# Kernel optimization log

Measured on AMD Instinct MI355X. Metric: run time of the kernel, lower is better.

The kernel has to match this reference:

```python
import jax, jax.numpy as jnp
import numpy as np

B, S, D, H, DFF = 2, 2048, 1024, 16, 4096
DK = D // H
EPS = 1e-5

def setup_inputs() -> dict:
    key = jax.random.key(0)
    ks = jax.random.split(key, 8)
    sc = lambda n: 1.0 / np.sqrt(n)
    return {
        "x": jax.random.normal(ks[0], (B, S, D), dtype=jnp.float32),
        "g1": jnp.ones((D,), dtype=jnp.float32),
        "g2": jnp.ones((D,), dtype=jnp.float32),
        "wq": jax.random.normal(ks[1], (D, D), dtype=jnp.float32) * sc(D),
        "wk": jax.random.normal(ks[2], (D, D), dtype=jnp.float32) * sc(D),
        "wv": jax.random.normal(ks[3], (D, D), dtype=jnp.float32) * sc(D),
        "wo": jax.random.normal(ks[4], (D, D), dtype=jnp.float32) * sc(D),
        "w1": jax.random.normal(ks[5], (DFF, D), dtype=jnp.float32) * sc(D),
        "w2": jax.random.normal(ks[6], (D, DFF), dtype=jnp.float32) * sc(DFF),
    }

def rmsnorm(a, g):
    norm = jnp.sqrt(jnp.mean(a * a, axis=-1, keepdims=True) + EPS)
    return a / norm * g

def gelu_erf(x):
    return x * 0.5 * (1.0 + jax.lax.erf(x * (1.0 / np.sqrt(2.0))))

def reference(x, g1, g2, wq, wk, wv, wo, w1, w2):
    b, s, d = x.shape
    h, dk = H, DK
    # --- attention sublayer (pre-norm) ---
    xn = rmsnorm(x, g1)
    # nn.Linear: y = x @ W.T ; reshape to [b, h, s, dk]
    q = (xn @ wq.T).reshape(b, s, h, dk).transpose(0, 2, 1, 3)
    k = (xn @ wk.T).reshape(b, s, h, dk).transpose(0, 2, 1, 3)
    v = (xn @ wv.T).reshape(b, s, h, dk).transpose(0, 2, 1, 3)
    scores = jnp.einsum('bhqd,bhkd->bhqk', q, k) / np.sqrt(dk).astype(np.float32)
    causal = jnp.triu(jnp.ones((s, s), dtype=bool), k=1)  # True above diagonal -> masked
    scores = jnp.where(causal, -jnp.inf, scores)
    weights = jax.nn.softmax(scores, axis=-1)
    attn = jnp.einsum('bhqk,bhkd->bhqd', weights, v)
    attn = attn.transpose(0, 2, 1, 3).reshape(b, s, d)
    x = x + attn @ wo.T
    # --- FFN sublayer (pre-norm) ---
    xn2 = rmsnorm(x, g2)
    ff = gelu_erf(xn2 @ w1.T) @ w2.T
    return x + ff
```

## Files before the change

### kernel.cpp

```cpp
#include <hip/hip_runtime.h>
#include <hip/hip_bf16.h>

typedef __attribute__((ext_vector_type(8))) short bf16x8;
typedef __attribute__((ext_vector_type(4))) float f32x4;

__device__ __forceinline__ unsigned short f2b(float f) {
    unsigned int u = __float_as_uint(f);
    unsigned int r = u + 0x7FFFu + ((u >> 16) & 1u);
    return (unsigned short)(r >> 16);
}

__device__ __forceinline__ float gelu_erf(float v) {
    return 0.5f * v * (1.0f + erff(v * 0.70710678118654752f));
}

__device__ __forceinline__ void gload_lds16(const void* g, void* l) {
    __builtin_amdgcn_global_load_lds(
        (const __attribute__((address_space(1))) void*)g,
        (__attribute__((address_space(3))) void*)l, 16, 0, 0);
}

__global__ void cast_bf16_k(const float* __restrict__ src, unsigned short* __restrict__ dst, int n4) {
    int i = blockIdx.x * blockDim.x + threadIdx.x;
    if (i < n4) {
        float4 v = ((const float4*)src)[i];
        ushort4 o;
        o.x = f2b(v.x); o.y = f2b(v.y); o.z = f2b(v.z); o.w = f2b(v.w);
        ((ushort4*)dst)[i] = o;
    }
}

__global__ void rmsnorm_bf16_k(const float* __restrict__ x, const float* __restrict__ g,
                               unsigned short* __restrict__ out) {
    int row = blockIdx.x;
    int t = threadIdx.x;
    const float4* xr = (const float4*)(x + (size_t)row * 1024);
    float4 xv = xr[t];
    float ss = xv.x * xv.x + xv.y * xv.y + xv.z * xv.z + xv.w * xv.w;
    #pragma unroll
    for (int off = 32; off; off >>= 1) ss += __shfl_xor(ss, off, 64);
    __shared__ float red[4];
    int wave = t >> 6, lane = t & 63;
    if (lane == 0) red[wave] = ss;
    __syncthreads();
    float tot = red[0] + red[1] + red[2] + red[3];
    float rn = rsqrtf(tot * (1.0f / 1024.0f) + 1e-5f);
    float4 gv = ((const float4*)g)[t];
    ushort4 o4;
    o4.x = f2b(xv.x * rn * gv.x);
    o4.y = f2b(xv.y * rn * gv.y);
    o4.z = f2b(xv.z * rn * gv.z);
    o4.w = f2b(xv.w * rn * gv.w);
    ((ushort4*)out)[(size_t)row * 256 + t] = o4;
}

__global__ void vtrans_k(const unsigned short* __restrict__ qkv, unsigned short* __restrict__ vt) {
    __shared__ unsigned short Ls[64 * 72];
    int st = blockIdx.x, bh = blockIdx.y, b = bh >> 4, h = bh & 15;
    int s0 = st * 64;
    int tid = threadIdx.x;
    const unsigned short* Vg = qkv + (size_t)(b * 2048 + s0) * 3072 + 2048 + h * 64;
    #pragma unroll
    for (int i = 0; i < 2; i++) {
        int idx = i * 256 + tid;
        int r = idx >> 3, c8 = (idx & 7) * 8;
        *(uint4*)&Ls[r * 72 + c8] = *(const uint4*)&Vg[(size_t)r * 3072 + c8];
    }
    __syncthreads();
    #pragma unroll
    for (int i = 0; i < 2; i++) {
        int idx = i * 256 + tid;
        int d = idx >> 3, s8 = (idx & 7) * 8;
        unsigned short tmp[8];
        #pragma unroll
        for (int j = 0; j < 8; j++) tmp[j] = Ls[(s8 + j) * 72 + d];
        *(uint4*)&vt[(size_t)(bh * 64 + d) * 2048 + s0 + s8] = *(uint4*)tmp;
    }
}

template <int EPI>
__launch_bounds__(256)
__global__ void gemm_bt(const unsigned short* __restrict__ A, const unsigned short* __restrict__ B,
                        const float* __restrict__ res, void* __restrict__ out,
                        int M, int N, int K) {
    __shared__ __align__(16) unsigned short smem[2 * 128 * 32];
    unsigned short* As = smem;
    unsigned short* Bs = smem + 128 * 32;

    int tid = threadIdx.x;
    int wave = tid >> 6, lane = tid & 63;
    int lrow = lane & 15, quad = lane >> 4;
    int qx8 = (quad ^ ((lrow >> 1) & 3)) * 8;

    int gx = gridDim.x, gy = gridDim.y;
    int cid = blockIdx.y * gx + blockIdx.x;
    int per = (gx * gy) >> 3;
    int nid = (cid & 7) * per + (cid >> 3);
    const int CG = 8;
    int group = nid / (CG * gy);
    int rem = nid % (CG * gy);
    int bxs = group * CG + (rem % CG);
    int bys = rem / CG;
    int bm = bys * 128, bn = bxs * 128;

    int wm = (wave & 1) * 64, wn = (wave >> 1) * 64;

    const unsigned short* Ab = A + (size_t)bm * K;
    const unsigned short* Bb = B + (size_t)bn * K;

    f32x4 zero = {0.f, 0.f, 0.f, 0.f};
    f32x4 acc[4][4];
    #pragma unroll
    for (int mi = 0; mi < 4; mi++)
        #pragma unroll
        for (int ni = 0; ni < 4; ni++) acc[mi][ni] = zero;

    int wbase = tid & 192;

    for (int k0 = 0; k0 < K; k0 += 32) {
        if (k0) __syncthreads();
        #pragma unroll
        for (int i = 0; i < 2; i++) {
            int idx = i * 256 + tid;
            int r = idx >> 2;
            int c = ((idx & 3) ^ ((idx >> 3) & 3)) * 8;
            gload_lds16(&Ab[(size_t)r * K + k0 + c], As + ((size_t)(i * 256 + wbase)) * 8);
            gload_lds16(&Bb[(size_t)r * K + k0 + c], Bs + ((size_t)(i * 256 + wbase)) * 8);
        }
        __syncthreads();

        bf16x8 af[4], bfr[4];
        #pragma unroll
        for (int mi = 0; mi < 4; mi++)
            af[mi] = *(const bf16x8*)&As[(wm + mi * 16 + lrow) * 32 + qx8];
        #pragma unroll
        for (int ni = 0; ni < 4; ni++)
            bfr[ni] = *(const bf16x8*)&Bs[(wn + ni * 16 + lrow) * 32 + qx8];
        #pragma unroll
        for (int mi = 0; mi < 4; mi++)
            #pragma unroll
            for (int ni = 0; ni < 4; ni++)
                acc[mi][ni] = __builtin_amdgcn_mfma_f32_16x16x32_bf16(af[mi], bfr[ni], acc[mi][ni], 0, 0, 0);
    }

    float* Cs = (float*)smem;
    int row16 = lane >> 2, cseg = (lane & 3) * 16;
    #pragma unroll
    for (int p = 0; p < 4; p++) {
        __syncthreads();
        #pragma unroll
        for (int ni = 0; ni < 4; ni++)
            #pragma unroll
            for (int r = 0; r < 4; r++)
                Cs[wave * 1024 + (quad * 4 + r) * 64 + ni * 16 + lrow] = acc[p][ni][r];
        __syncthreads();
        const float* src = &Cs[wave * 1024 + row16 * 64 + cseg];
        int grow = bm + wm + p * 16 + row16;
        int gcol = bn + wn + cseg;
        size_t off = (size_t)grow * N + gcol;
        if (EPI == 1) {
            float* op = (float*)out + off;
            const float* rp = res + off;
            #pragma unroll
            for (int j = 0; j < 4; j++) {
                float4 v = ((const float4*)src)[j];
                float4 rr = ((const float4*)rp)[j];
                v.x += rr.x; v.y += rr.y; v.z += rr.z; v.w += rr.w;
                ((float4*)op)[j] = v;
            }
        } else {
            unsigned short tmp[16];
            #pragma unroll
            for (int j = 0; j < 16; j++) {
                float v = src[j];
                if (EPI == 2) v = gelu_erf(v);
                tmp[j] = f2b(v);
            }
            unsigned short* op = (unsigned short*)out + off;
            *(uint4*)op = *(uint4*)tmp;
            *(uint4*)(op + 8) = *(uint4*)(tmp + 8);
        }
    }
}

__launch_bounds__(256)
__global__ void gemm_bt64(const unsigned short* __restrict__ A, const unsigned short* __restrict__ B,
                          const float* __restrict__ res, float* __restrict__ out,
                          int M, int N, int K) {
    __shared__ __align__(16) unsigned short As[128 * 32];
    __shared__ __align__(16) unsigned short Bs[64 * 32];

    int tid = threadIdx.x, wave = tid >> 6, lane = tid & 63;
    int lrow = lane & 15, quad = lane >> 4;
    int qx8 = (quad ^ ((lrow >> 1) & 3)) * 8;

    int gx = gridDim.x, gy = gridDim.y;
    int cid = blockIdx.y * gx + blockIdx.x;
    int per = (gx * gy) >> 3;
    int nid = (cid & 7) * per + (cid >> 3);
    const int CG = 8;
    int group = nid / (CG * gy);
    int rem = nid % (CG * gy);
    int bxs = group * CG + (rem % CG);
    int bys = rem / CG;
    int bm = bys * 128, bn = bxs * 64;

    int wm = (wave & 1) * 64, wn = (wave >> 1) * 32;

    f32x4 zero = {0.f, 0.f, 0.f, 0.f};
    f32x4 acc[4][2];
    #pragma unroll
    for (int mi = 0; mi < 4; mi++)
        #pragma unroll
        for (int ni = 0; ni < 2; ni++) acc[mi][ni] = zero;

    int rr4 = lane >> 2;
    int c8s = ((lane & 3) ^ ((lane >> 3) & 3)) * 8;
    const unsigned short* Ab = A + (size_t)(bm + wave * 32 + rr4) * K + c8s;
    const unsigned short* Bb = B + (size_t)(bn + wave * 16 + rr4) * K + c8s;

    for (int k0 = 0; k0 < K; k0 += 32) {
        if (k0) __syncthreads();
        gload_lds16(Ab + k0, &As[(wave * 32) * 32]);
        gload_lds16(Ab + (size_t)16 * K + k0, &As[(wave * 32 + 16) * 32]);
        gload_lds16(Bb + k0, &Bs[(wave * 16) * 32]);
        __syncthreads();

        bf16x8 af[4], bfr[2];
        #pragma unroll
        for (int mi = 0; mi < 4; mi++)
            af[mi] = *(const bf16x8*)&As[(wm + mi * 16 + lrow) * 32 + qx8];
        #pragma unroll
        for (int ni = 0; ni < 2; ni++)
            bfr[ni] = *(const bf16x8*)&Bs[(wn + ni * 16 + lrow) * 32 + qx8];
        #pragma unroll
        for (int mi = 0; mi < 4; mi++)
            #pragma unroll
            for (int ni = 0; ni < 2; ni++)
                acc[mi][ni] = __builtin_amdgcn_mfma_f32_16x16x32_bf16(af[mi], bfr[ni], acc[mi][ni], 0, 0, 0);
    }

    float* Cs = (float*)As;
    int row16 = lane >> 2, cseg = (lane & 3) * 8;
    #pragma unroll
    for (int p = 0; p < 4; p++) {
        __syncthreads();
        #pragma unroll
        for (int ni = 0; ni < 2; ni++)
            #pragma unroll
            for (int r = 0; r < 4; r++)
                Cs[wave * 512 + (quad * 4 + r) * 32 + ni * 16 + lrow] = acc[p][ni][r];
        __syncthreads();
        const float* src = &Cs[wave * 512 + row16 * 32 + cseg];
        int grow = bm + wm + p * 16 + row16;
        int gcol = bn + wn + cseg;
        size_t off = (size_t)grow * N + gcol;
        float* op = out + off;
        const float* rp = res + off;
        #pragma unroll
        for (int j = 0; j < 2; j++) {
            float4 v = ((const float4*)src)[j];
            float4 rv = ((const float4*)rp)[j];
            v.x += rv.x; v.y += rv.y; v.z += rv.z; v.w += rv.w;
            ((float4*)op)[j] = v;
        }
    }
}

__launch_bounds__(256)
__global__ void attn_k(const unsigned short* __restrict__ qkv,
                       const unsigned short* __restrict__ vt,
                       unsigned short* __restrict__ attn_out) {
    const int ROWQKV = 3072;
    int qt = (int)(gridDim.x - 1 - blockIdx.x);
    int bh = blockIdx.y;
    int b = bh >> 4, h = bh & 15;
    int q0 = qt * 128;

    __shared__ __align__(16) unsigned short Ks[2][2][64 * 32];
    __shared__ __align__(16) unsigned short Vs[2][2][64 * 32];
    __shared__ __align__(16) unsigned short Ps[8][16 * 72];

    int tid = threadIdx.x, wave = tid >> 6, lane = tid & 63;
    int lrow = lane & 15, quad = lane >> 4;
    int rr4 = lane >> 2;
    int c8s = ((lane & 3) ^ ((lane >> 3) & 3)) * 8;
    int qx8 = (quad ^ ((lrow >> 1) & 3)) * 8;

    size_t base = (size_t)b * 2048 * ROWQKV;

    const unsigned short* QgA = qkv + base + (size_t)(q0 + wave * 16 + lrow) * ROWQKV + h * 64 + quad * 8;
    bf16x8 aA0 = *(const bf16x8*)QgA;
    bf16x8 aA1 = *(const bf16x8*)(QgA + 32);
    const unsigned short* QgB = QgA + (size_t)64 * ROWQKV;
    bf16x8 aB0 = *(const bf16x8*)QgB;
    bf16x8 aB1 = *(const bf16x8*)(QgB + 32);

    const unsigned short* Kg0 = qkv + base + (size_t)(wave * 16 + rr4) * ROWQKV + 1024 + h * 64 + c8s;
    const unsigned short* Vg0 = vt + (size_t)(bh * 64 + wave * 16 + rr4) * 2048 + c8s;

    f32x4 zero = {0.f, 0.f, 0.f, 0.f};
    f32x4 oA[4], oB[4];
    float lA[4], lB[4];
    #pragma unroll
    for (int ni = 0; ni < 4; ni++) { oA[ni] = zero; oB[ni] = zero; }
    #pragma unroll
    for (int r = 0; r < 4; r++) { lA[r] = 0.f; lB[r] = 0.f; }

    const float C = 0.18033688011112042f;

    unsigned short* PwA = Ps[wave];
    unsigned short* PwB = Ps[wave + 4];

    gload_lds16(Kg0,      &Ks[0][0][wave * 16 * 32]);
    gload_lds16(Kg0 + 32, &Ks[0][1][wave * 16 * 32]);
    gload_lds16(Vg0,      &Vs[0][0][wave * 16 * 32]);
    gload_lds16(Vg0 + 32, &Vs[0][1][wave * 16 * 32]);

    auto process = [&](bf16x8 a0, bf16x8 a1, f32x4* o, float* l,
                       unsigned short* Pw, bool diag, int buf) {
        f32x4 s[4];
        #pragma unroll
        for (int ni = 0; ni < 4; ni++) s[ni] = zero;
        #pragma unroll
        for (int ni = 0; ni < 4; ni++) {
            bf16x8 bb = *(const bf16x8*)&Ks[buf][0][(ni * 16 + lrow) * 32 + qx8];
            s[ni] = __builtin_amdgcn_mfma_f32_16x16x32_bf16(a0, bb, s[ni], 0, 0, 0);
        }
        #pragma unroll
        for (int ni = 0; ni < 4; ni++) {
            bf16x8 bb = *(const bf16x8*)&Ks[buf][1][(ni * 16 + lrow) * 32 + qx8];
            s[ni] = __builtin_amdgcn_mfma_f32_16x16x32_bf16(a1, bb, s[ni], 0, 0, 0);
        }
        if (diag) {
            #pragma unroll
            for (int r = 0; r < 4; r++)
                #pragma unroll
                for (int ni = 0; ni < 4; ni++) {
                    float p = exp2f(s[ni][r] * C);
                    if (ni * 16 + lrow > wave * 16 + quad * 4 + r) p = 0.f;
                    s[ni][r] = p;
                    l[r] += p;
                }
        } else {
            #pragma unroll
            for (int r = 0; r < 4; r++)
                #pragma unroll
                for (int ni = 0; ni < 4; ni++) {
                    float p = exp2f(s[ni][r] * C);
                    s[ni][r] = p;
                    l[r] += p;
                }
        }
        #pragma unroll
        for (int ni = 0; ni < 4; ni++)
            #pragma unroll
            for (int r = 0; r < 4; r++)
                Pw[(quad * 4 + r) * 72 + ni * 16 + lrow] = f2b(s[ni][r]);
        bf16x8 p0 = *(const bf16x8*)&Pw[lrow * 72 + quad * 8];
        bf16x8 p1 = *(const bf16x8*)&Pw[lrow * 72 + 32 + quad * 8];
        #pragma unroll
        for (int ni = 0; ni < 4; ni++) {
            bf16x8 bb = *(const bf16x8*)&Vs[buf][0][(ni * 16 + lrow) * 32 + qx8];
            o[ni] = __builtin_amdgcn_mfma_f32_16x16x32_bf16(p0, bb, o[ni], 0, 0, 0);
        }
        #pragma unroll
        for (int ni = 0; ni < 4; ni++) {
            bf16x8 bb = *(const bf16x8*)&Vs[buf][1][(ni * 16 + lrow) * 32 + qx8];
            o[ni] = __builtin_amdgcn_mfma_f32_16x16x32_bf16(p1, bb, o[ni], 0, 0, 0);
        }
    };

    int nkt = 2 * qt + 2;
    for (int kt = 0; kt < nkt; kt++) {
        __syncthreads();
        if (kt + 1 < nkt) {
            int nb = (kt + 1) & 1;
            const unsigned short* Kg = Kg0 + (size_t)(kt + 1) * 64 * ROWQKV;
            const unsigned short* Vg = Vg0 + (size_t)(kt + 1) * 64;
            gload_lds16(Kg,      &Ks[nb][0][wave * 16 * 32]);
            gload_lds16(Kg + 32, &Ks[nb][1][wave * 16 * 32]);
            gload_lds16(Vg,      &Vs[nb][0][wave * 16 * 32]);
            gload_lds16(Vg + 32, &Vs[nb][1][wave * 16 * 32]);
        }
        int buf = kt & 1;
        if (kt < nkt - 1) process(aA0, aA1, oA, lA, PwA, kt == nkt - 2, buf);
        process(aB0, aB1, oB, lB, PwB, kt == nkt - 1, buf);
    }

    #pragma unroll
    for (int r = 0; r < 4; r++) {
        #pragma unroll
        for (int off = 1; off < 16; off <<= 1) {
            lA[r] += __shfl_xor(lA[r], off, 64);
            lB[r] += __shfl_xor(lB[r], off, 64);
        }
    }

    #pragma unroll
    for (int strip = 0; strip < 2; strip++) {
        f32x4* o = strip ? oB : oA;
        float* l = strip ? lB : lA;
        #pragma unroll
        for (int r = 0; r < 4; r++) {
            float inv = 1.0f / l[r];
            int q = q0 + strip * 64 + wave * 16 + quad * 4 + r;
            #pragma unroll
            for (int ni = 0; ni < 4; ni++)
                attn_out[((size_t)b * 2048 + q) * 1024 + h * 64 + ni * 16 + lrow] = f2b(o[ni][r] * inv);
        }
    }
}

extern "C" void kernel_launch(void* const* d_in, const int* in_sizes, int n_in,
                              void* d_out, int out_size, void* d_ws, size_t ws_size,
                              hipStream_t stream) {
    const float* x  = (const float*)d_in[0];
    const float* g1 = (const float*)d_in[1];
    const float* g2 = (const float*)d_in[2];
    const float* wq = (const float*)d_in[3];
    const float* wk = (const float*)d_in[4];
    const float* wv = (const float*)d_in[5];
    const float* wo = (const float*)d_in[6];
    const float* w1 = (const float*)d_in[7];
    const float* w2 = (const float*)d_in[8];
    float* out = (float*)d_out;

    const size_t BS = 4096;
    const size_t D = 1024, DFF = 4096;

    char* w = (char*)d_ws;
    unsigned short* xn_b   = (unsigned short*)w; w += BS * D * 2;
    unsigned short* wqkv_b = (unsigned short*)w; w += 3 * D * D * 2;
    unsigned short* qkv_b  = (unsigned short*)w; w += BS * 3 * D * 2;
    unsigned short* vt_b   = (unsigned short*)w; w += BS * D * 2;
    unsigned short* attn_b = (unsigned short*)w; w += BS * D * 2;
    unsigned short* wo_b   = (unsigned short*)w; w += D * D * 2;
    float*          x2     = (float*)w;          w += BS * D * 4;
    unsigned short* xn2_b  = (unsigned short*)w; w += BS * D * 2;
    unsigned short* w1_b   = (unsigned short*)w; w += DFF * D * 2;
    unsigned short* h_b    = (unsigned short*)w; w += BS * DFF * 2;
    unsigned short* w2_b   = (unsigned short*)w; w += D * DFF * 2;

    int nW = (int)(D * D / 4);
    cast_bf16_k<<<(nW + 255) / 256, 256, 0, stream>>>(wq, wqkv_b, nW);
    cast_bf16_k<<<(nW + 255) / 256, 256, 0, stream>>>(wk, wqkv_b + D * D, nW);
    cast_bf16_k<<<(nW + 255) / 256, 256, 0, stream>>>(wv, wqkv_b + 2 * D * D, nW);
    cast_bf16_k<<<(nW + 255) / 256, 256, 0, stream>>>(wo, wo_b, nW);
    int nF = (int)(DFF * D / 4);
    cast_bf16_k<<<(nF + 255) / 256, 256, 0, stream>>>(w1, w1_b, nF);
    cast_bf16_k<<<(nF + 255) / 256, 256, 0, stream>>>(w2, w2_b, nF);

    rmsnorm_bf16_k<<<(int)BS, 256, 0, stream>>>(x, g1, xn_b);

    gemm_bt<0><<<dim3(24, 32), 256, 0, stream>>>(xn_b, wqkv_b, nullptr, qkv_b, 4096, 3072, 1024);

    vtrans_k<<<dim3(32, 32), 256, 0, stream>>>(qkv_b, vt_b);

    attn_k<<<dim3(16, 32), 256, 0, stream>>>(qkv_b, vt_b, attn_b);

    gemm_bt64<<<dim3(16, 32), 256, 0, stream>>>(attn_b, wo_b, x, x2, 4096, 1024, 1024);

    rmsnorm_bf16_k<<<(int)BS, 256, 0, stream>>>(x2, g2, xn2_b);

    gemm_bt<2><<<dim3(32, 32), 256, 0, stream>>>(xn2_b, w1_b, nullptr, h_b, 4096, 4096, 1024);

    gemm_bt64<<<dim3(16, 32), 256, 0, stream>>>(h_b, w2_b, x2, out, 4096, 1024, 4096);
}
```

Before: 393.4 us.

## Load attention K/V fragments directly from global, halve query tile, fold scale into Wq

```diff
diff --git a/kernel.cpp b/kernel.cpp
--- a/kernel.cpp
+++ b/kernel.cpp
@@ -20,12 +20,14 @@
         (__attribute__((address_space(3))) void*)l, 16, 0, 0);
 }
 
-__global__ void cast_bf16_k(const float* __restrict__ src, unsigned short* __restrict__ dst, int n4) {
+__global__ void cast_bf16_k(const float* __restrict__ src, unsigned short* __restrict__ dst,
+                            int n4, float scale) {
     int i = blockIdx.x * blockDim.x + threadIdx.x;
     if (i < n4) {
         float4 v = ((const float4*)src)[i];
         ushort4 o;
-        o.x = f2b(v.x); o.y = f2b(v.y); o.z = f2b(v.z); o.w = f2b(v.w);
+        o.x = f2b(v.x * scale); o.y = f2b(v.y * scale);
+        o.z = f2b(v.z * scale); o.w = f2b(v.w * scale);
         ((ushort4*)dst)[i] = o;
     }
 }
@@ -275,140 +277,108 @@
     int qt = (int)(gridDim.x - 1 - blockIdx.x);
     int bh = blockIdx.y;
     int b = bh >> 4, h = bh & 15;
-    int q0 = qt * 128;
-
-    __shared__ __align__(16) unsigned short Ks[2][2][64 * 32];
-    __shared__ __align__(16) unsigned short Vs[2][2][64 * 32];
-    __shared__ __align__(16) unsigned short Ps[8][16 * 72];
+    int q0 = qt * 64;
+
+    __shared__ __align__(16) unsigned short Ps[4][16 * 72];
 
     int tid = threadIdx.x, wave = tid >> 6, lane = tid & 63;
     int lrow = lane & 15, quad = lane >> 4;
-    int rr4 = lane >> 2;
-    int c8s = ((lane & 3) ^ ((lane >> 3) & 3)) * 8;
-    int qx8 = (quad ^ ((lrow >> 1) & 3)) * 8;
 
     size_t base = (size_t)b * 2048 * ROWQKV;
 
-    const unsigned short* QgA = qkv + base + (size_t)(q0 + wave * 16 + lrow) * ROWQKV + h * 64 + quad * 8;
-    bf16x8 aA0 = *(const bf16x8*)QgA;
-    bf16x8 aA1 = *(const bf16x8*)(QgA + 32);
-    const unsigned short* QgB = QgA + (size_t)64 * ROWQKV;
-    bf16x8 aB0 = *(const bf16x8*)QgB;
-    bf16x8 aB1 = *(const bf16x8*)(QgB + 32);
-
-    const unsigned short* Kg0 = qkv + base + (size_t)(wave * 16 + rr4) * ROWQKV + 1024 + h * 64 + c8s;
-    const unsigned short* Vg0 = vt + (size_t)(bh * 64 + wave * 16 + rr4) * 2048 + c8s;
+    const unsigned short* Qg = qkv + base + (size_t)(q0 + wave * 16 + lrow) * ROWQKV + h * 64 + quad * 8;
+    bf16x8 qf0 = *(const bf16x8*)Qg;
+    bf16x8 qf1 = *(const bf16x8*)(Qg + 32);
+
+    const unsigned short* Kg = qkv + base + (size_t)lrow * ROWQKV + 1024 + h * 64 + quad * 8;
+    const unsigned short* Vg = vt + (size_t)(bh * 64 + lrow) * 2048 + quad * 8;
 
     f32x4 zero = {0.f, 0.f, 0.f, 0.f};
-    f32x4 oA[4], oB[4];
-    float lA[4], lB[4];
-    #pragma unroll
-    for (int ni = 0; ni < 4; ni++) { oA[ni] = zero; oB[ni] = zero; }
-    #pragma unroll
-    for (int r = 0; r < 4; r++) { lA[r] = 0.f; lB[r] = 0.f; }
-
-    const float C = 0.18033688011112042f;
-
-    unsigned short* PwA = Ps[wave];
-    unsigned short* PwB = Ps[wave + 4];
-
-    gload_lds16(Kg0,      &Ks[0][0][wave * 16 * 32]);
-    gload_lds16(Kg0 + 32, &Ks[0][1][wave * 16 * 32]);
-    gload_lds16(Vg0,      &Vs[0][0][wave * 16 * 32]);
-    gload_lds16(Vg0 + 32, &Vs[0][1][wave * 16 * 32]);
-
-    auto process = [&](bf16x8 a0, bf16x8 a1, f32x4* o, float* l,
-                       unsigned short* Pw, bool diag, int buf) {
+    f32x4 o[4];
+    #pragma unroll
+    for (int ni = 0; ni < 4; ni++) o[ni] = zero;
+    float l = 0.f;
+
+    unsigned short* Pw = Ps[wave];
+    int qloc = wave * 16 + lrow;
+
+    for (int kt = 0; kt <= qt; kt++) {
+        const unsigned short* Kt = Kg + (size_t)(kt * 64) * ROWQKV;
+        const unsigned short* Vt = Vg + kt * 64;
+
+        bf16x8 kf[4][2];
+        #pragma unroll
+        for (int ni = 0; ni < 4; ni++) {
+            kf[ni][0] = *(const bf16x8*)(Kt + (size_t)(ni * 16) * ROWQKV);
+            kf[ni][1] = *(const bf16x8*)(Kt + (size_t)(ni * 16) * ROWQKV + 32);
+        }
+        bf16x8 vf[4][2];
+        #pragma unroll
+        for (int ni = 0; ni < 4; ni++) {
+            vf[ni][0] = *(const bf16x8*)(Vt + (size_t)(ni * 16) * 2048);
+            vf[ni][1] = *(const bf16x8*)(Vt + (size_t)(ni * 16) * 2048 + 32);
+        }
+
         f32x4 s[4];
         #pragma unroll
         for (int ni = 0; ni < 4; ni++) s[ni] = zero;
         #pragma unroll
-        for (int ni = 0; ni < 4; ni++) {
-            bf16x8 bb = *(const bf16x8*)&Ks[buf][0][(ni * 16 + lrow) * 32 + qx8];
-            s[ni] = __builtin_amdgcn_mfma_f32_16x16x32_bf16(a0, bb, s[ni], 0, 0, 0);
-        }
-        #pragma unroll
-        for (int ni = 0; ni < 4; ni++) {
-            bf16x8 bb = *(const bf16x8*)&Ks[buf][1][(ni * 16 + lrow) * 32 + qx8];
-            s[ni] = __builtin_amdgcn_mfma_f32_16x16x32_bf16(a1, bb, s[ni], 0, 0, 0);
-        }
-        if (diag) {
-            #pragma unroll
-            for (int r = 0; r < 4; r++)
+        for (int ni = 0; ni < 4; ni++)
+            s[ni] = __builtin_amdgcn_mfma_f32_16x16x32_bf16(kf[ni][0], qf0, s[ni], 0, 0, 0);
+        #pragma unroll
+        for (int ni = 0; ni < 4; ni++)
+            s[ni] = __builtin_amdgcn_mfma_f32_16x16x32_bf16(kf[ni][1], qf1, s[ni], 0, 0, 0);
+
+        if (kt == qt) {
+            #pragma unroll
+            for (int ni = 0; ni < 4; ni++)
                 #pragma unroll
-                for (int ni = 0; ni < 4; ni++) {
-                    float p = exp2f(s[ni][r] * C);
-                    if (ni * 16 + lrow > wave * 16 + quad * 4 + r) p = 0.f;
+                for (int r = 0; r < 4; r++) {
+                    float p = exp2f(s[ni][r]);
+                    if (ni * 16 + quad * 4 + r > qloc) p = 0.f;
                     s[ni][r] = p;
-                    l[r] += p;
+                    l += p;
                 }
         } else {
             #pragma unroll
-            for (int r = 0; r < 4; r++)
+            for (int ni = 0; ni < 4; ni++)
                 #pragma unroll
-                for (int ni = 0; ni < 4; ni++) {
-                    float p = exp2f(s[ni][r] * C);
+                for (int r = 0; r < 4; r++) {
+                    float p = exp2f(s[ni][r]);
                     s[ni][r] = p;
-                    l[r] += p;
+                    l += p;
                 }
         }
-        #pragma unroll
-        for (int ni = 0; ni < 4; ni++)
-            #pragma unroll
-            for (int r = 0; r < 4; r++)
-                Pw[(quad * 4 + r) * 72 + ni * 16 + lrow] = f2b(s[ni][r]);
+
+        #pragma unroll
+        for (int ni = 0; ni < 4; ni++) {
+            uint2 pk;
+            pk.x = (unsigned int)f2b(s[ni][0]) | ((unsigned int)f2b(s[ni][1]) << 16);
+            pk.y = (unsigned int)f2b(s[ni][2]) | ((unsigned int)f2b(s[ni][3]) << 16);
+            *(uint2*)&Pw[lrow * 72 + ni * 16 + quad * 4] = pk;
+        }
         bf16x8 p0 = *(const bf16x8*)&Pw[lrow * 72 + quad * 8];
         bf16x8 p1 = *(const bf16x8*)&Pw[lrow * 72 + 32 + quad * 8];
-        #pragma unroll
-        for (int ni = 0; ni < 4; ni++) {
-            bf16x8 bb = *(const bf16x8*)&Vs[buf][0][(ni * 16 + lrow) * 32 + qx8];
-            o[ni] = __builtin_amdgcn_mfma_f32_16x16x32_bf16(p0, bb, o[ni], 0, 0, 0);
-        }
-        #pragma unroll
-        for (int ni = 0; ni < 4; ni++) {
-            bf16x8 bb = *(const bf16x8*)&Vs[buf][1][(ni * 16 + lrow) * 32 + qx8];
-            o[ni] = __builtin_amdgcn_mfma_f32_16x16x32_bf16(p1, bb, o[ni], 0, 0, 0);
-        }
-    };
-
-    int nkt = 2 * qt + 2;
-    for (int kt = 0; kt < nkt; kt++) {
-        __syncthreads();
-        if (kt + 1 < nkt) {
-            int nb = (kt + 1) & 1;
-            const unsigned short* Kg = Kg0 + (size_t)(kt + 1) * 64 * ROWQKV;
-            const unsigned short* Vg = Vg0 + (size_t)(kt + 1) * 64;
-            gload_lds16(Kg,      &Ks[nb][0][wave * 16 * 32]);
-            gload_lds16(Kg + 32, &Ks[nb][1][wave * 16 * 32]);
-            gload_lds16(Vg,      &Vs[nb][0][wave * 16 * 32]);
-            gload_lds16(Vg + 32, &Vs[nb][1][wave * 16 * 32]);
-        }
-        int buf = kt & 1;
-        if (kt < nkt - 1) process(aA0, aA1, oA, lA, PwA, kt == nkt - 2, buf);
-        process(aB0, aB1, oB, lB, PwB, kt == nkt - 1, buf);
-    }
+
+        #pragma unroll
+        for (int ni = 0; ni < 4; ni++)
+            o[ni] = __builtin_amdgcn_mfma_f32_16x16x32_bf16(p0, vf[ni][0], o[ni], 0, 0, 0);
+        #pragma unroll
+        for (int ni = 0; ni < 4; ni++)
+            o[ni] = __builtin_amdgcn_mfma_f32_16x16x32_bf16(p1, vf[ni][1], o[ni], 0, 0, 0);
+    }
+
+    l += __shfl_xor(l, 16, 64);
+    l += __shfl_xor(l, 32, 64);
 
     #pragma unroll
     for (int r = 0; r < 4; r++) {
-        #pragma unroll
-        for (int off = 1; off < 16; off <<= 1) {
-            lA[r] += __shfl_xor(lA[r], off, 64);
-            lB[r] += __shfl_xor(lB[r], off, 64);
-        }
-    }
-
-    #pragma unroll
-    for (int strip = 0; strip < 2; strip++) {
-        f32x4* o = strip ? oB : oA;
-        float* l = strip ? lB : lA;
-        #pragma unroll
-        for (int r = 0; r < 4; r++) {
-            float inv = 1.0f / l[r];
-            int q = q0 + strip * 64 + wave * 16 + quad * 4 + r;
-            #pragma unroll
-            for (int ni = 0; ni < 4; ni++)
-                attn_out[((size_t)b * 2048 + q) * 1024 + h * 64 + ni * 16 + lrow] = f2b(o[ni][r] * inv);
-        }
+        float lr = __shfl(l, quad * 4 + r, 64);
+        float inv = 1.0f / lr;
+        int q = q0 + wave * 16 + quad * 4 + r;
+        #pragma unroll
+        for (int ni = 0; ni < 4; ni++)
+            attn_out[((size_t)b * 2048 + q) * 1024 + h * 64 + ni * 16 + lrow] = f2b(o[ni][r] * inv);
     }
 }
 
@@ -428,6 +398,7 @@
 
     const size_t BS = 4096;
     const size_t D = 1024, DFF = 4096;
+    const float QSCALE = 0.18033688011112042f;
 
     char* w = (char*)d_ws;
     unsigned short* xn_b   = (unsigned short*)w; w += BS * D * 2;
@@ -443,13 +414,13 @@
     unsigned short* w2_b   = (unsigned short*)w; w += D * DFF * 2;
 
     int nW = (int)(D * D / 4);
-    cast_bf16_k<<<(nW + 255) / 256, 256, 0, stream>>>(wq, wqkv_b, nW);
-    cast_bf16_k<<<(nW + 255) / 256, 256, 0, stream>>>(wk, wqkv_b + D * D, nW);
-    cast_bf16_k<<<(nW + 255) / 256, 256, 0, stream>>>(wv, wqkv_b + 2 * D * D, nW);
-    cast_bf16_k<<<(nW + 255) / 256, 256, 0, stream>>>(wo, wo_b, nW);
+    cast_bf16_k<<<(nW + 255) / 256, 256, 0, stream>>>(wq, wqkv_b, nW, QSCALE);
+    cast_bf16_k<<<(nW + 255) / 256, 256, 0, stream>>>(wk, wqkv_b + D * D, nW, 1.0f);
+    cast_bf16_k<<<(nW + 255) / 256, 256, 0, stream>>>(wv, wqkv_b + 2 * D * D, nW, 1.0f);
+    cast_bf16_k<<<(nW + 255) / 256, 256, 0, stream>>>(wo, wo_b, nW, 1.0f);
     int nF = (int)(DFF * D / 4);
-    cast_bf16_k<<<(nF + 255) / 256, 256, 0, stream>>>(w1, w1_b, nF);
-    cast_bf16_k<<<(nF + 255) / 256, 256, 0, stream>>>(w2, w2_b, nF);
+    cast_bf16_k<<<(nF + 255) / 256, 256, 0, stream>>>(w1, w1_b, nF, 1.0f);
+    cast_bf16_k<<<(nF + 255) / 256, 256, 0, stream>>>(w2, w2_b, nF, 1.0f);
 
     rmsnorm_bf16_k<<<(int)BS, 256, 0, stream>>>(x, g1, xn_b);
 
@@ -457,7 +428,7 @@
 
     vtrans_k<<<dim3(32, 32), 256, 0, stream>>>(qkv_b, vt_b);
 
-    attn_k<<<dim3(16, 32), 256, 0, stream>>>(qkv_b, vt_b, attn_b);
+    attn_k<<<dim3(32, 32), 256, 0, stream>>>(qkv_b, vt_b, attn_b);
 
     gemm_bt64<<<dim3(16, 32), 256, 0, stream>>>(attn_b, wo_b, x, x2, 4096, 1024, 1024);
 
```

Result: slower. 537.5 us (+36.6%).
